# Performance work log

Hardware: AMD Instinct MI355X
Metric: run time of the kernel (lower is better)

## Reference

```python
import jax, jax.numpy as jnp
import numpy as np

N_EXPERTS = 8
TOP_K = 2
AUX_COEF = 0.01
Z_COEF = 0.001


def setup_inputs() -> dict:
    key = jax.random.key(0)
    ks = jax.random.split(key, 5)
    B, S, D, F, E = 2, 2048, 768, 2048, N_EXPERTS
    std = 0.02
    std_out = std / np.sqrt(2 * 12)  # scale_init_by_depth, n_layers=12
    return {
        "x": jax.random.normal(ks[0], (B, S, D), jnp.float32),
        "router_w": jax.random.normal(ks[1], (D, E), jnp.float32) * std,
        "w1": jax.random.normal(ks[2], (E, D, F), jnp.float32) * std,
        "w2": jax.random.normal(ks[3], (E, F, D), jnp.float32) * std_out,
        "w3": jax.random.normal(ks[4], (E, D, F), jnp.float32) * std,
    }


def reference(x, router_w, w1, w2, w3):
    B, S, D = x.shape
    E = w1.shape[0]
    x_flat = x.reshape(-1, D)                      # [N, D]
    n_tokens = x_flat.shape[0]

    router_logits = x_flat @ router_w               # [N, E]
    probs = jax.nn.softmax(router_logits.astype(jnp.float32), axis=-1)
    topk_w, topk_i = jax.lax.top_k(probs, TOP_K)    # [N, K]
    topk_w = topk_w / jnp.sum(topk_w, axis=-1, keepdims=True)

    # Combine: equivalent to sort/group dispatch + per-expert GEMM + index_add,
    # expressed as a masked per-expert (fixed, small E) dense pass.
    out = jnp.zeros((n_tokens, D), dtype=x.dtype)
    for e in range(E):
        gate = jnp.sum(jnp.where(topk_i == e, topk_w, 0.0), axis=-1)  # [N] f32
        h = jax.nn.silu(x_flat @ w1[e]) * (x_flat @ w3[e])            # [N, F]
        out = out + gate[:, None].astype(x.dtype) * (h @ w2[e])

    # Switch-style load-balancing aux loss + z-loss
    importance = probs.mean(axis=0)                 # [E]
    top1 = topk_i[:, 0]
    load = jnp.zeros((E,), jnp.float32).at[top1].add(1.0) / n_tokens
    aux_loss = E * jnp.sum(importance * load) * AUX_COEF
    z_loss = jnp.mean(router_logits.astype(jnp.float32) ** 2) * Z_COEF

    return out.reshape(B, S, D), aux_loss, z_loss
```

## Files before the change

kernel.cpp:

```cpp
#include <hip/hip_runtime.h>
#include <hip/hip_bf16.h>

constexpr int NT = 4096;
constexpr int DD = 768;
constexpr int FF = 2048;
constexpr int NE = 8;
constexpr int MAXROWS = 8704;
constexpr int MAXTILES = 136;

constexpr int IDX_CNTA   = 0;
constexpr int IDX_CNTT1  = 8;
constexpr int IDX_CUR    = 16;
constexpr int IDX_IMP    = 24;
constexpr int IDX_ZSUM   = 32;
constexpr int IDX_NTILES = 33;
constexpr int IDX_OFF    = 34;
constexpr int IDX_EXPT   = 48;

constexpr size_t OFF_META   = 0;
constexpr size_t OFF_TKE    = 1024;
constexpr size_t OFF_GATE   = OFF_TKE    + (size_t)NT*2*4;
constexpr size_t OFF_ROWOF  = OFF_GATE   + (size_t)NT*2*4;
constexpr size_t OFF_TOKROW = OFF_ROWOF  + (size_t)NT*2*4;
constexpr size_t OFF_XG     = 134144;
constexpr size_t OFF_W1T    = OFF_XG  + (size_t)MAXROWS*DD*2;
constexpr size_t OFF_W3T    = OFF_W1T + (size_t)NE*FF*DD*2;
constexpr size_t OFF_W2T    = OFF_W3T + (size_t)NE*FF*DD*2;
constexpr size_t OFF_H      = OFF_W2T + (size_t)NE*FF*DD*2;
constexpr size_t OFF_OP     = OFF_H   + (size_t)MAXROWS*FF*2;

typedef float f32x4 __attribute__((ext_vector_type(4)));
typedef __bf16 bf16x8v __attribute__((ext_vector_type(8)));

__device__ inline unsigned short f2bf_bits(float f) {
  __bf16 h = (__bf16)f;
  return *(unsigned short*)&h;
}
__device__ inline float bf2f(unsigned short u) {
  unsigned v = (unsigned)u << 16;
  return *(float*)&v;
}

constexpr int RB = 128;
__global__ __launch_bounds__(256) void router_kernel(const float* __restrict__ x,
    const float* __restrict__ rw, int* __restrict__ meta,
    int* __restrict__ tke, float* __restrict__ gateArr) {
  __shared__ float s_imp[NE];
  __shared__ float s_z;
  __shared__ int s_cnt1[NE], s_cnta[NE];
  if (threadIdx.x < NE) { s_imp[threadIdx.x] = 0.f; s_cnt1[threadIdx.x] = 0; s_cnta[threadIdx.x] = 0; }
  if (threadIdx.x == 0) s_z = 0.f;
  __syncthreads();

  const int wave = threadIdx.x >> 6, lane = threadIdx.x & 63;
  float impacc[NE];
  #pragma unroll
  for (int e = 0; e < NE; ++e) impacc[e] = 0.f;
  float zacc = 0.f;

  for (int t = blockIdx.x * 4 + wave; t < NT; t += RB * 4) {
    float acc[NE];
    #pragma unroll
    for (int e = 0; e < NE; ++e) acc[e] = 0.f;
    const float* xr = x + (size_t)t * DD;
    for (int i = lane; i < DD; i += 64) {
      float xv = xr[i];
      const float* r = rw + i * NE;
      #pragma unroll
      for (int e = 0; e < NE; ++e) acc[e] += xv * r[e];
    }
    #pragma unroll
    for (int off = 32; off > 0; off >>= 1) {
      #pragma unroll
      for (int e = 0; e < NE; ++e) acc[e] += __shfl_xor(acc[e], off);
    }
    float mx = acc[0];
    #pragma unroll
    for (int e = 1; e < NE; ++e) mx = fmaxf(mx, acc[e]);
    float p[NE]; float s = 0.f;
    #pragma unroll
    for (int e = 0; e < NE; ++e) { p[e] = __expf(acc[e] - mx); s += p[e]; }
    float inv = 1.f / s;
    #pragma unroll
    for (int e = 0; e < NE; ++e) p[e] *= inv;
    int e0 = 0; float p0 = p[0];
    #pragma unroll
    for (int e = 1; e < NE; ++e) if (p[e] > p0) { p0 = p[e]; e0 = e; }
    int e1 = -1; float p1 = -1.f;
    #pragma unroll
    for (int e = 0; e < NE; ++e) if (e != e0 && p[e] > p1) { p1 = p[e]; e1 = e; }
    if (lane == 0) {
      #pragma unroll
      for (int e = 0; e < NE; ++e) { impacc[e] += p[e]; zacc += acc[e] * acc[e]; }
      atomicAdd(&s_cnt1[e0], 1);
      atomicAdd(&s_cnta[e0], 1);
      atomicAdd(&s_cnta[e1], 1);
      float gs = 1.f / (p0 + p1);
      tke[t*2]   = e0; tke[t*2+1] = e1;
      gateArr[t*2] = p0 * gs; gateArr[t*2+1] = p1 * gs;
    }
  }
  if (lane == 0) {
    #pragma unroll
    for (int e = 0; e < NE; ++e) atomicAdd(&s_imp[e], impacc[e]);
    atomicAdd(&s_z, zacc);
  }
  __syncthreads();
  float* fmeta = (float*)meta;
  if (threadIdx.x < NE) {
    atomicAdd(&fmeta[IDX_IMP + threadIdx.x], s_imp[threadIdx.x]);
    atomicAdd(&meta[IDX_CNTT1 + threadIdx.x], s_cnt1[threadIdx.x]);
    atomicAdd(&meta[IDX_CNTA + threadIdx.x], s_cnta[threadIdx.x]);
  }
  if (threadIdx.x == NE) atomicAdd(&fmeta[IDX_ZSUM], s_z);
}

__global__ void scan_kernel(int* __restrict__ meta, float* __restrict__ out_tail) {
  if (threadIdx.x != 0 || blockIdx.x != 0) return;
  float* fmeta = (float*)meta;
  int off = 0, tidx = 0;
  for (int e = 0; e < NE; ++e) {
    meta[IDX_OFF + e] = off;
    int ntile = (meta[IDX_CNTA + e] + 63) >> 6;
    for (int i = 0; i < ntile; ++i) meta[IDX_EXPT + tidx++] = e;
    off += ntile << 6;
  }
  meta[IDX_OFF + NE] = off;
  meta[IDX_NTILES] = tidx;
  float aux = 0.f;
  for (int e = 0; e < NE; ++e)
    aux += (fmeta[IDX_IMP + e] / (float)NT) * ((float)meta[IDX_CNTT1 + e] / (float)NT);
  out_tail[0] = (float)NE * aux * 0.01f;
  out_tail[1] = fmeta[IDX_ZSUM] / (float)(NT * NE) * 0.001f;
}

__global__ __launch_bounds__(256) void scatter_kernel(const int* __restrict__ tke,
    int* __restrict__ meta, int* __restrict__ rowof, int* __restrict__ tokrow) {
  __shared__ int s_cnt[NE], s_base[NE];
  const int t = blockIdx.x * 256 + threadIdx.x;
  if (threadIdx.x < NE) s_cnt[threadIdx.x] = 0;
  __syncthreads();
  const int e0 = tke[t*2], e1 = tke[t*2 + 1];
  const int l0 = atomicAdd(&s_cnt[e0], 1);
  const int l1 = atomicAdd(&s_cnt[e1], 1);
  __syncthreads();
  if (threadIdx.x < NE)
    s_base[threadIdx.x] = atomicAdd(&meta[IDX_CUR + threadIdx.x], s_cnt[threadIdx.x]);
  __syncthreads();
  const int r0 = meta[IDX_OFF + e0] + s_base[e0] + l0;
  const int r1 = meta[IDX_OFF + e1] + s_base[e1] + l1;
  rowof[t*2]     = r0;
  rowof[t*2 + 1] = r1;
  tokrow[r0] = t;
  tokrow[r1] = t;
}

__global__ __launch_bounds__(192) void gather_kernel(const float* __restrict__ x,
    const int* __restrict__ tokrow, const int* __restrict__ meta,
    __bf16* __restrict__ Xg) {
  const int row = blockIdx.x;
  if (row >= meta[IDX_OFF + NE]) return;
  const int tok = tokrow[row];
  ushort4* dst = (ushort4*)(Xg + (size_t)row * DD);
  const int i = threadIdx.x;
  ushort4 o;
  if (tok >= 0) {
    float4 v = ((const float4*)(x + (size_t)tok * DD))[i];
    o.x = f2bf_bits(v.x); o.y = f2bf_bits(v.y);
    o.z = f2bf_bits(v.z); o.w = f2bf_bits(v.w);
  } else {
    o.x = o.y = o.z = o.w = 0;
  }
  dst[i] = o;
}

__global__ __launch_bounds__(256) void transpose_cvt(const float* __restrict__ src,
    __bf16* __restrict__ dst, int R, int C) {
  const size_t eoff = (size_t)blockIdx.z * R * C;
  src += eoff; dst += eoff;
  const int r0 = blockIdx.y * 64, c0 = blockIdx.x * 64;
  __shared__ __bf16 tile[64 * 65];
  const int t = threadIdx.x;
  #pragma unroll
  for (int i = 0; i < 16; ++i) {
    int idx = t + i * 256; int r = idx >> 6, c = idx & 63;
    tile[r * 65 + c] = (__bf16)src[(size_t)(r0 + r) * C + c0 + c];
  }
  __syncthreads();
  #pragma unroll
  for (int i = 0; i < 16; ++i) {
    int idx = t + i * 256; int c = idx >> 6, r = idx & 63;
    dst[(size_t)(c0 + c) * R + r0 + r] = tile[r * 65 + c];
  }
}

__global__ __launch_bounds__(256) void gemm1_kernel(const __bf16* __restrict__ Xg,
    const __bf16* __restrict__ W1t, const __bf16* __restrict__ W3t,
    __bf16* __restrict__ Hb, const int* __restrict__ meta) {
  const int mt = blockIdx.y;
  if (mt >= meta[IDX_NTILES]) return;
  const int e = meta[IDX_EXPT + mt];
  const int n0 = blockIdx.x * 64;
  const int m0 = mt * 64;
  __shared__ __align__(16) __bf16 As[64*32], B1s[64*32], B3s[64*32];
  const int t = threadIdx.x, wave = t >> 6, lane = t & 63;
  const int sr = t >> 2, sc = (t & 3) * 8;
  const __bf16* w1e = W1t + (size_t)e * FF * DD;
  const __bf16* w3e = W3t + (size_t)e * FF * DD;
  const f32x4 zero = {0.f, 0.f, 0.f, 0.f};
  f32x4 acc1[4] = {zero, zero, zero, zero};
  f32x4 acc3[4] = {zero, zero, zero, zero};
  for (int k0 = 0; k0 < DD; k0 += 32) {
    *(bf16x8v*)&As[sr*32 + sc]  = *(const bf16x8v*)&Xg [(size_t)(m0 + sr)*DD + k0 + sc];
    *(bf16x8v*)&B1s[sr*32 + sc] = *(const bf16x8v*)&w1e[(size_t)(n0 + sr)*DD + k0 + sc];
    *(bf16x8v*)&B3s[sr*32 + sc] = *(const bf16x8v*)&w3e[(size_t)(n0 + sr)*DD + k0 + sc];
    __syncthreads();
    bf16x8v a = *(const bf16x8v*)&As[(wave*16 + (lane & 15))*32 + (lane >> 4)*8];
    #pragma unroll
    for (int s = 0; s < 4; ++s) {
      bf16x8v b1 = *(const bf16x8v*)&B1s[(s*16 + (lane & 15))*32 + (lane >> 4)*8];
      bf16x8v b3 = *(const bf16x8v*)&B3s[(s*16 + (lane & 15))*32 + (lane >> 4)*8];
      acc1[s] = __builtin_amdgcn_mfma_f32_16x16x32_bf16(a, b1, acc1[s], 0, 0, 0);
      acc3[s] = __builtin_amdgcn_mfma_f32_16x16x32_bf16(a, b3, acc3[s], 0, 0, 0);
    }
    __syncthreads();
  }
  const int rowb = m0 + wave*16 + (lane >> 4)*4;
  const int colb = n0 + (lane & 15);
  #pragma unroll
  for (int s = 0; s < 4; ++s) {
    #pragma unroll
    for (int r = 0; r < 4; ++r) {
      float c1 = acc1[s][r], c3 = acc3[s][r];
      float h = c1 / (1.f + __expf(-c1)) * c3;
      Hb[(size_t)(rowb + r)*FF + colb + s*16] = (__bf16)h;
    }
  }
}

__global__ __launch_bounds__(256) void gemm2_kernel(const __bf16* __restrict__ Hb,
    const __bf16* __restrict__ W2t, __bf16* __restrict__ OP,
    const int* __restrict__ meta) {
  const int mt = blockIdx.y;
  if (mt >= meta[IDX_NTILES]) return;
  const int e = meta[IDX_EXPT + mt];
  const int n0 = blockIdx.x * 64;
  const int m0 = mt * 64;
  __shared__ __align__(16) __bf16 As[64*32], Bs[64*32];
  const int t = threadIdx.x, wave = t >> 6, lane = t & 63;
  const int sr = t >> 2, sc = (t & 3) * 8;
  const __bf16* w2e = W2t + (size_t)e * DD * FF;
  const f32x4 zero = {0.f, 0.f, 0.f, 0.f};
  f32x4 acc[4] = {zero, zero, zero, zero};
  for (int k0 = 0; k0 < FF; k0 += 32) {
    *(bf16x8v*)&As[sr*32 + sc] = *(const bf16x8v*)&Hb [(size_t)(m0 + sr)*FF + k0 + sc];
    *(bf16x8v*)&Bs[sr*32 + sc] = *(const bf16x8v*)&w2e[(size_t)(n0 + sr)*FF + k0 + sc];
    __syncthreads();
    bf16x8v a = *(const bf16x8v*)&As[(wave*16 + (lane & 15))*32 + (lane >> 4)*8];
    #pragma unroll
    for (int s = 0; s < 4; ++s) {
      bf16x8v b = *(const bf16x8v*)&Bs[(s*16 + (lane & 15))*32 + (lane >> 4)*8];
      acc[s] = __builtin_amdgcn_mfma_f32_16x16x32_bf16(a, b, acc[s], 0, 0, 0);
    }
    __syncthreads();
  }
  const int rowb = m0 + wave*16 + (lane >> 4)*4;
  const int colb = n0 + (lane & 15);
  #pragma unroll
  for (int s = 0; s < 4; ++s) {
    #pragma unroll
    for (int r = 0; r < 4; ++r)
      OP[(size_t)(rowb + r)*DD + colb + s*16] = (__bf16)acc[s][r];
  }
}

__global__ __launch_bounds__(192) void combine_kernel(const __bf16* __restrict__ OP,
    const int* __restrict__ rowof, const float* __restrict__ gateArr,
    float* __restrict__ out) {
  const int t = blockIdx.x;
  const int r0 = rowof[t*2], r1 = rowof[t*2 + 1];
  const float g0 = gateArr[t*2], g1 = gateArr[t*2 + 1];
  const ushort4* p0 = (const ushort4*)(OP + (size_t)r0 * DD);
  const ushort4* p1 = (const ushort4*)(OP + (size_t)r1 * DD);
  const int i = threadIdx.x;
  ushort4 a = p0[i], b = p1[i];
  float4 o;
  o.x = g0 * bf2f(a.x) + g1 * bf2f(b.x);
  o.y = g0 * bf2f(a.y) + g1 * bf2f(b.y);
  o.z = g0 * bf2f(a.z) + g1 * bf2f(b.z);
  o.w = g0 * bf2f(a.w) + g1 * bf2f(b.w);
  ((float4*)(out + (size_t)t * DD))[i] = o;
}

extern "C" void kernel_launch(void* const* d_in, const int* in_sizes, int n_in,
                              void* d_out, int out_size, void* d_ws, size_t ws_size,
                              hipStream_t stream) {
  const float* x  = (const float*)d_in[0];
  const float* rw = (const float*)d_in[1];
  const float* w1 = (const float*)d_in[2];
  const float* w2 = (const float*)d_in[3];
  const float* w3 = (const float*)d_in[4];
  float* out = (float*)d_out;

  char* ws = (char*)d_ws;
  int*    meta   = (int*)(ws + OFF_META);
  int*    tke    = (int*)(ws + OFF_TKE);
  float*  gateA  = (float*)(ws + OFF_GATE);
  int*    rowof  = (int*)(ws + OFF_ROWOF);
  int*    tokrow = (int*)(ws + OFF_TOKROW);
  __bf16* Xg     = (__bf16*)(ws + OFF_XG);
  __bf16* W1t    = (__bf16*)(ws + OFF_W1T);
  __bf16* W3t    = (__bf16*)(ws + OFF_W3T);
  __bf16* W2t    = (__bf16*)(ws + OFF_W2T);
  __bf16* Hb     = (__bf16*)(ws + OFF_H);
  __bf16* OP     = (__bf16*)(ws + OFF_OP);

  hipMemsetAsync(ws + OFF_META, 0, 1024, stream);
  hipMemsetAsync(ws + OFF_TOKROW, 0xFF, (size_t)MAXROWS * 4, stream);

  transpose_cvt<<<dim3(FF/64, DD/64, NE), 256, 0, stream>>>(w1, W1t, DD, FF);
  transpose_cvt<<<dim3(FF/64, DD/64, NE), 256, 0, stream>>>(w3, W3t, DD, FF);
  transpose_cvt<<<dim3(DD/64, FF/64, NE), 256, 0, stream>>>(w2, W2t, FF, DD);

  router_kernel<<<RB, 256, 0, stream>>>(x, rw, meta, tke, gateA);
  scan_kernel<<<1, 64, 0, stream>>>(meta, out + (size_t)NT * DD);
  scatter_kernel<<<NT/256, 256, 0, stream>>>(tke, meta, rowof, tokrow);
  gather_kernel<<<MAXROWS, 192, 0, stream>>>(x, tokrow, meta, Xg);

  gemm1_kernel<<<dim3(FF/64, MAXTILES), 256, 0, stream>>>(Xg, W1t, W3t, Hb, meta);
  gemm2_kernel<<<dim3(DD/64, MAXTILES), 256, 0, stream>>>(Hb, W2t, OP, meta);
  combine_kernel<<<NT, 192, 0, stream>>>(OP, rowof, gateA, out);
}
```

Before: 428.2 us.

## Enlarge MoE GEMM tiles to 128 rows and stage operands via global_load_lds

Expert row padding goes from 64 to 128, so both grouped GEMMs use 128-row M tiles. gemm2 also uses 128-wide N tiles with a 2x2 wave layout. Operand tiles are copied straight from global memory into LDS with global_load_lds, which skips the register round-trip. The three weight transpose launches become one fused launch with paired 32-bit stores. The aim is more reuse per LDS load and fewer launches, at the cost of more padded rows, higher register use and fewer blocks in gemm2.

```diff
diff --git a/kernel.cpp b/kernel.cpp
--- a/kernel.cpp
+++ b/kernel.cpp
@@ -5,8 +5,8 @@
 constexpr int DD = 768;
 constexpr int FF = 2048;
 constexpr int NE = 8;
-constexpr int MAXROWS = 8704;
-constexpr int MAXTILES = 136;
+constexpr int MAXROWS = 9216;
+constexpr int MAXMT128 = 72;
 
 constexpr int IDX_CNTA   = 0;
 constexpr int IDX_CNTT1  = 8;
@@ -22,7 +22,7 @@
 constexpr size_t OFF_GATE   = OFF_TKE    + (size_t)NT*2*4;
 constexpr size_t OFF_ROWOF  = OFF_GATE   + (size_t)NT*2*4;
 constexpr size_t OFF_TOKROW = OFF_ROWOF  + (size_t)NT*2*4;
-constexpr size_t OFF_XG     = 134144;
+constexpr size_t OFF_XG     = 136448;
 constexpr size_t OFF_W1T    = OFF_XG  + (size_t)MAXROWS*DD*2;
 constexpr size_t OFF_W3T    = OFF_W1T + (size_t)NE*FF*DD*2;
 constexpr size_t OFF_W2T    = OFF_W3T + (size_t)NE*FF*DD*2;
@@ -39,6 +39,12 @@
 __device__ inline float bf2f(unsigned short u) {
   unsigned v = (unsigned)u << 16;
   return *(float*)&v;
+}
+
+__device__ __forceinline__ void glds16(const void* g, void* l) {
+  __builtin_amdgcn_global_load_lds(
+      (const __attribute__((address_space(1))) unsigned int*)g,
+      (__attribute__((address_space(3))) unsigned int*)l, 16, 0, 0);
 }
 
 constexpr int RB = 128;
@@ -121,9 +127,9 @@
   int off = 0, tidx = 0;
   for (int e = 0; e < NE; ++e) {
     meta[IDX_OFF + e] = off;
-    int ntile = (meta[IDX_CNTA + e] + 63) >> 6;
+    int ntile = (meta[IDX_CNTA + e] + 127) >> 7;
     for (int i = 0; i < ntile; ++i) meta[IDX_EXPT + tidx++] = e;
-    off += ntile << 6;
+    off += ntile << 7;
   }
   meta[IDX_OFF + NE] = off;
   meta[IDX_NTILES] = tidx;
@@ -174,11 +180,17 @@
   dst[i] = o;
 }
 
-__global__ __launch_bounds__(256) void transpose_cvt(const float* __restrict__ src,
-    __bf16* __restrict__ dst, int R, int C) {
-  const size_t eoff = (size_t)blockIdx.z * R * C;
-  src += eoff; dst += eoff;
-  const int r0 = blockIdx.y * 64, c0 = blockIdx.x * 64;
+__global__ __launch_bounds__(256) void transpose_cvt_all(
+    const float* __restrict__ w1, const float* __restrict__ w3,
+    const float* __restrict__ w2, __bf16* __restrict__ W1t,
+    __bf16* __restrict__ W3t, __bf16* __restrict__ W2t) {
+  const int z = blockIdx.z, which = z >> 3, e = z & 7;
+  const float* src; __bf16* dst; int R, C, rt, ct;
+  if (which == 0)      { src = w1; dst = W1t; R = DD; C = FF; rt = blockIdx.y; ct = blockIdx.x; }
+  else if (which == 1) { src = w3; dst = W3t; R = DD; C = FF; rt = blockIdx.y; ct = blockIdx.x; }
+  else                 { src = w2; dst = W2t; R = FF; C = DD; rt = blockIdx.x; ct = blockIdx.y; }
+  src += (size_t)e * DD * FF; dst += (size_t)e * DD * FF;
+  const int r0 = rt * 64, c0 = ct * 64;
   __shared__ __bf16 tile[64 * 65];
   const int t = threadIdx.x;
   #pragma unroll
@@ -188,9 +200,12 @@
   }
   __syncthreads();
   #pragma unroll
-  for (int i = 0; i < 16; ++i) {
-    int idx = t + i * 256; int c = idx >> 6, r = idx & 63;
-    dst[(size_t)(c0 + c) * R + r0 + r] = tile[r * 65 + c];
+  for (int i = 0; i < 8; ++i) {
+    int idx = t + i * 256; int c = idx >> 5, rp = idx & 31;
+    ushort2 o;
+    o.x = *(unsigned short*)&tile[(rp*2    ) * 65 + c];
+    o.y = *(unsigned short*)&tile[(rp*2 + 1) * 65 + c];
+    *(ushort2*)&dst[(size_t)(c0 + c) * R + r0 + rp*2] = o;
   }
 }
 
@@ -201,39 +216,62 @@
   if (mt >= meta[IDX_NTILES]) return;
   const int e = meta[IDX_EXPT + mt];
   const int n0 = blockIdx.x * 64;
-  const int m0 = mt * 64;
-  __shared__ __align__(16) __bf16 As[64*32], B1s[64*32], B3s[64*32];
+  const int m0 = mt * 128;
+  __shared__ __align__(16) __bf16 As[128*32], B1s[64*32], B3s[64*32];
   const int t = threadIdx.x, wave = t >> 6, lane = t & 63;
-  const int sr = t >> 2, sc = (t & 3) * 8;
   const __bf16* w1e = W1t + (size_t)e * FF * DD;
   const __bf16* w3e = W3t + (size_t)e * FF * DD;
   const f32x4 zero = {0.f, 0.f, 0.f, 0.f};
-  f32x4 acc1[4] = {zero, zero, zero, zero};
-  f32x4 acc3[4] = {zero, zero, zero, zero};
+  f32x4 acc1[2][4], acc3[2][4];
+  #pragma unroll
+  for (int i = 0; i < 2; ++i)
+    #pragma unroll
+    for (int j = 0; j < 4; ++j) { acc1[i][j] = zero; acc3[i][j] = zero; }
+
+  const __bf16* gA  = Xg  + (size_t)(m0 + 32*wave + (lane >> 2)) * DD + (lane & 3) * 8;
+  const __bf16* gB1 = w1e + (size_t)(n0 + 16*wave + (lane >> 2)) * DD + (lane & 3) * 8;
+  const __bf16* gB3 = w3e + (size_t)(n0 + 16*wave + (lane >> 2)) * DD + (lane & 3) * 8;
+  __bf16* lA0 = &As [(32*wave     ) * 32];
+  __bf16* lA1 = &As [(32*wave + 16) * 32];
+  __bf16* lB1 = &B1s[(16*wave     ) * 32];
+  __bf16* lB3 = &B3s[(16*wave     ) * 32];
+
   for (int k0 = 0; k0 < DD; k0 += 32) {
-    *(bf16x8v*)&As[sr*32 + sc]  = *(const bf16x8v*)&Xg [(size_t)(m0 + sr)*DD + k0 + sc];
-    *(bf16x8v*)&B1s[sr*32 + sc] = *(const bf16x8v*)&w1e[(size_t)(n0 + sr)*DD + k0 + sc];
-    *(bf16x8v*)&B3s[sr*32 + sc] = *(const bf16x8v*)&w3e[(size_t)(n0 + sr)*DD + k0 + sc];
+    glds16(gA  + k0,           lA0);
+    glds16(gA  + k0 + 16*DD,   lA1);
+    glds16(gB1 + k0,           lB1);
+    glds16(gB3 + k0,           lB3);
     __syncthreads();
-    bf16x8v a = *(const bf16x8v*)&As[(wave*16 + (lane & 15))*32 + (lane >> 4)*8];
-    #pragma unroll
-    for (int s = 0; s < 4; ++s) {
-      bf16x8v b1 = *(const bf16x8v*)&B1s[(s*16 + (lane & 15))*32 + (lane >> 4)*8];
-      bf16x8v b3 = *(const bf16x8v*)&B3s[(s*16 + (lane & 15))*32 + (lane >> 4)*8];
-      acc1[s] = __builtin_amdgcn_mfma_f32_16x16x32_bf16(a, b1, acc1[s], 0, 0, 0);
-      acc3[s] = __builtin_amdgcn_mfma_f32_16x16x32_bf16(a, b3, acc3[s], 0, 0, 0);
-    }
+    bf16x8v a[2], b1[4], b3[4];
+    #pragma unroll
+    for (int i = 0; i < 2; ++i)
+      a[i] = *(const bf16x8v*)&As[(32*wave + 16*i + (lane & 15))*32 + (lane >> 4)*8];
+    #pragma unroll
+    for (int j = 0; j < 4; ++j) {
+      b1[j] = *(const bf16x8v*)&B1s[(16*j + (lane & 15))*32 + (lane >> 4)*8];
+      b3[j] = *(const bf16x8v*)&B3s[(16*j + (lane & 15))*32 + (lane >> 4)*8];
+    }
+    #pragma unroll
+    for (int i = 0; i < 2; ++i)
+      #pragma unroll
+      for (int j = 0; j < 4; ++j) {
+        acc1[i][j] = __builtin_amdgcn_mfma_f32_16x16x32_bf16(a[i], b1[j], acc1[i][j], 0, 0, 0);
+        acc3[i][j] = __builtin_amdgcn_mfma_f32_16x16x32_bf16(a[i], b3[j], acc3[i][j], 0, 0, 0);
+      }
     __syncthreads();
   }
-  const int rowb = m0 + wave*16 + (lane >> 4)*4;
-  const int colb = n0 + (lane & 15);
-  #pragma unroll
-  for (int s = 0; s < 4; ++s) {
-    #pragma unroll
-    for (int r = 0; r < 4; ++r) {
-      float c1 = acc1[s][r], c3 = acc3[s][r];
-      float h = c1 / (1.f + __expf(-c1)) * c3;
-      Hb[(size_t)(rowb + r)*FF + colb + s*16] = (__bf16)h;
+  #pragma unroll
+  for (int i = 0; i < 2; ++i) {
+    const int rowb = m0 + 32*wave + 16*i + (lane >> 4)*4;
+    #pragma unroll
+    for (int j = 0; j < 4; ++j) {
+      const int col = n0 + 16*j + (lane & 15);
+      #pragma unroll
+      for (int r = 0; r < 4; ++r) {
+        float c1 = acc1[i][j][r], c3 = acc3[i][j][r];
+        float h = c1 / (1.f + __expf(-c1)) * c3;
+        Hb[(size_t)(rowb + r)*FF + col] = (__bf16)h;
+      }
     }
   }
 }
@@ -244,33 +282,55 @@
   const int mt = blockIdx.y;
   if (mt >= meta[IDX_NTILES]) return;
   const int e = meta[IDX_EXPT + mt];
-  const int n0 = blockIdx.x * 64;
-  const int m0 = mt * 64;
-  __shared__ __align__(16) __bf16 As[64*32], Bs[64*32];
+  const int n0 = blockIdx.x * 128;
+  const int m0 = mt * 128;
+  __shared__ __align__(16) __bf16 As[128*32], Bs[128*32];
   const int t = threadIdx.x, wave = t >> 6, lane = t & 63;
-  const int sr = t >> 2, sc = (t & 3) * 8;
+  const int wm = wave & 1, wn = wave >> 1;
   const __bf16* w2e = W2t + (size_t)e * DD * FF;
   const f32x4 zero = {0.f, 0.f, 0.f, 0.f};
-  f32x4 acc[4] = {zero, zero, zero, zero};
+  f32x4 acc[4][4];
+  #pragma unroll
+  for (int i = 0; i < 4; ++i)
+    #pragma unroll
+    for (int j = 0; j < 4; ++j) acc[i][j] = zero;
+
+  const __bf16* gA = Hb  + (size_t)(m0 + 32*wave + (lane >> 2)) * FF + (lane & 3) * 8;
+  const __bf16* gB = w2e + (size_t)(n0 + 32*wave + (lane >> 2)) * FF + (lane & 3) * 8;
+  __bf16* lA0 = &As[(32*wave     ) * 32];
+  __bf16* lA1 = &As[(32*wave + 16) * 32];
+  __bf16* lB0 = &Bs[(32*wave     ) * 32];
+  __bf16* lB1 = &Bs[(32*wave + 16) * 32];
+
   for (int k0 = 0; k0 < FF; k0 += 32) {
-    *(bf16x8v*)&As[sr*32 + sc] = *(const bf16x8v*)&Hb [(size_t)(m0 + sr)*FF + k0 + sc];
-    *(bf16x8v*)&Bs[sr*32 + sc] = *(const bf16x8v*)&w2e[(size_t)(n0 + sr)*FF + k0 + sc];
+    glds16(gA + k0,          lA0);
+    glds16(gA + k0 + 16*FF,  lA1);
+    glds16(gB + k0,          lB0);
+    glds16(gB + k0 + 16*FF,  lB1);
     __syncthreads();
-    bf16x8v a = *(const bf16x8v*)&As[(wave*16 + (lane & 15))*32 + (lane >> 4)*8];
-    #pragma unroll
-    for (int s = 0; s < 4; ++s) {
-      bf16x8v b = *(const bf16x8v*)&Bs[(s*16 + (lane & 15))*32 + (lane >> 4)*8];
-      acc[s] = __builtin_amdgcn_mfma_f32_16x16x32_bf16(a, b, acc[s], 0, 0, 0);
-    }
+    bf16x8v a[4], b[4];
+    #pragma unroll
+    for (int i = 0; i < 4; ++i) {
+      a[i] = *(const bf16x8v*)&As[(64*wm + 16*i + (lane & 15))*32 + (lane >> 4)*8];
+      b[i] = *(const bf16x8v*)&Bs[(64*wn + 16*i + (lane & 15))*32 + (lane >> 4)*8];
+    }
+    #pragma unroll
+    for (int i = 0; i < 4; ++i)
+      #pragma unroll
+      for (int j = 0; j < 4; ++j)
+        acc[i][j] = __builtin_amdgcn_mfma_f32_16x16x32_bf16(a[i], b[j], acc[i][j], 0, 0, 0);
     __syncthreads();
   }
-  const int rowb = m0 + wave*16 + (lane >> 4)*4;
-  const int colb = n0 + (lane & 15);
-  #pragma unroll
-  for (int s = 0; s < 4; ++s) {
-    #pragma unroll
-    for (int r = 0; r < 4; ++r)
-      OP[(size_t)(rowb + r)*DD + colb + s*16] = (__bf16)acc[s][r];
+  #pragma unroll
+  for (int i = 0; i < 4; ++i) {
+    const int rowb = m0 + 64*wm + 16*i + (lane >> 4)*4;
+    #pragma unroll
+    for (int j = 0; j < 4; ++j) {
+      const int col = n0 + 64*wn + 16*j + (lane & 15);
+      #pragma unroll
+      for (int r = 0; r < 4; ++r)
+        OP[(size_t)(rowb + r)*DD + col] = (__bf16)acc[i][j][r];
+    }
   }
 }
 
@@ -318,16 +378,14 @@
   hipMemsetAsync(ws + OFF_META, 0, 1024, stream);
   hipMemsetAsync(ws + OFF_TOKROW, 0xFF, (size_t)MAXROWS * 4, stream);
 
-  transpose_cvt<<<dim3(FF/64, DD/64, NE), 256, 0, stream>>>(w1, W1t, DD, FF);
-  transpose_cvt<<<dim3(FF/64, DD/64, NE), 256, 0, stream>>>(w3, W3t, DD, FF);
-  transpose_cvt<<<dim3(DD/64, FF/64, NE), 256, 0, stream>>>(w2, W2t, FF, DD);
+  transpose_cvt_all<<<dim3(32, 12, 24), 256, 0, stream>>>(w1, w3, w2, W1t, W3t, W2t);
 
   router_kernel<<<RB, 256, 0, stream>>>(x, rw, meta, tke, gateA);
   scan_kernel<<<1, 64, 0, stream>>>(meta, out + (size_t)NT * DD);
   scatter_kernel<<<NT/256, 256, 0, stream>>>(tke, meta, rowof, tokrow);
   gather_kernel<<<MAXROWS, 192, 0, stream>>>(x, tokrow, meta, Xg);
 
-  gemm1_kernel<<<dim3(FF/64, MAXTILES), 256, 0, stream>>>(Xg, W1t, W3t, Hb, meta);
-  gemm2_kernel<<<dim3(DD/64, MAXTILES), 256, 0, stream>>>(Hb, W2t, OP, meta);
+  gemm1_kernel<<<dim3(FF/64, MAXMT128), 256, 0, stream>>>(Xg, W1t, W3t, Hb, meta);
+  gemm2_kernel<<<dim3(DD/128, MAXMT128), 256, 0, stream>>>(Hb, W2t, OP, meta);
   combine_kernel<<<NT, 192, 0, stream>>>(OP, rowof, gateA, out);
 }
```

Result: faster. 382.1 us (-10.8%).
